# Kernel optimization log

Measured on AMD Instinct MI355X. Metric: run time of the kernel, lower is better.

Reference implementation:

```python
import jax, jax.numpy as jnp
import numpy as np

B, NMASK, DIM, HEADS = 8, 1024, 768, 12
HEAD_DIM = DIM // HEADS
SCALE = HEAD_DIM ** -0.5
NEG = -1e9  # finite stand-in for -inf to keep fully-masked rows NaN-free


def setup_inputs() -> dict:
    key = jax.random.key(0)
    ks = jax.random.split(key, 7)
    x = jax.random.normal(ks[0], (B, NMASK + 1, DIM), dtype=jnp.float32)
    # valid-prefix padding mask (realistic variable-length batch), lengths >= 1
    lengths = jax.random.randint(ks[1], (B,), 1, NMASK + 1)
    mask = jnp.arange(NMASK)[None, :] < lengths[:, None]  # (B, NMASK) bool
    w_qkv = jax.random.normal(ks[2], (DIM, 3 * DIM), dtype=jnp.float32) * (DIM ** -0.5)
    b_qkv = jax.random.normal(ks[3], (3 * DIM,), dtype=jnp.float32) * 0.02
    w_proj = jax.random.normal(ks[4], (DIM, DIM), dtype=jnp.float32) * (DIM ** -0.5)
    b_proj = jax.random.normal(ks[5], (DIM,), dtype=jnp.float32) * 0.02
    return {"x": x, "mask": mask, "w_qkv": w_qkv, "b_qkv": b_qkv,
            "w_proj": w_proj, "b_proj": b_proj}


def reference(x, mask, w_qkv, b_qkv, w_proj, b_proj):
    b, n, _ = x.shape
    qkv = x @ w_qkv + b_qkv                        # (b, n, 3*dim)
    qkv = qkv.reshape(b, n, 3, HEADS, HEAD_DIM)    # 'b n (qkv h d)'
    qkv = jnp.transpose(qkv, (2, 0, 3, 1, 4))      # (3, b, h, n, d)
    q, k, v = qkv[0], qkv[1], qkv[2]
    logits = jnp.einsum('bhid,bhjd->bhij', q, k) * SCALE
    m = jnp.pad(mask, ((0, 0), (1, 0)), constant_values=True)   # prepend CLS=True
    am = m[:, None, :] & m[:, :, None]             # (b, n, n)
    logits = jnp.where(am[:, None, :, :], logits, NEG)
    attn = jax.nn.softmax(logits, axis=-1)
    out = jnp.einsum('bhij,bhjd->bhid', attn, v)   # (b, h, n, d)
    out = jnp.transpose(out, (0, 2, 1, 3)).reshape(b, n, DIM)
    return out @ w_proj + b_proj                   # dropout is identity (eval/p=0)
```

## Files before the change

kernel.cpp:

```cpp
#include <hip/hip_runtime.h>
#include <stdint.h>

#define BATCH   8
#define NMASK_  1024
#define SEQ     1025
#define NPAD    1056
#define DIM     768
#define HEADS   12
#define HD      64
#define BHN     (BATCH*HEADS)
#define MROWS   (BATCH*SEQ)
#define K3      (3*DIM)

typedef unsigned short u16;
typedef __attribute__((ext_vector_type(8))) short s8v;
typedef __attribute__((ext_vector_type(4))) float f4v;
typedef __attribute__((ext_vector_type(4))) unsigned short u16x4;

__device__ __forceinline__ u16 rne_bf16(float f) {
  unsigned u = __float_as_uint(f);
  u += 0x7fffu + ((u >> 16) & 1u);
  return (u16)(u >> 16);
}
__device__ __forceinline__ float bf2f(u16 u) {
  return __uint_as_float(((unsigned)u) << 16);
}

__device__ __forceinline__ void gld16(const u16* g, u16* l) {
  __builtin_amdgcn_global_load_lds(
      (const __attribute__((address_space(1))) void*)g,
      (__attribute__((address_space(3))) void*)l, 16, 0, 0);
}

__global__ __launch_bounds__(256) void k_len(const int* __restrict__ mask,
                                             int* __restrict__ lens) {
  int b = blockIdx.x, t = threadIdx.x;
  int s = 0;
  for (int j = t; j < NMASK_; j += 256) s += (mask[b * NMASK_ + j] != 0) ? 1 : 0;
  __shared__ int red[256];
  red[t] = s; __syncthreads();
  for (int st = 128; st > 0; st >>= 1) { if (t < st) red[t] += red[t + st]; __syncthreads(); }
  if (t == 0) lens[b] = red[0] + 1;
}

__global__ __launch_bounds__(256) void k_cvt_x(const float* __restrict__ x,
                                               u16* __restrict__ xb, int n4) {
  int i = blockIdx.x * 256 + threadIdx.x;
  if (i >= n4) return;
  float4 v = ((const float4*)x)[i];
  u16x4 o;
  o[0] = rne_bf16(v.x); o[1] = rne_bf16(v.y); o[2] = rne_bf16(v.z); o[3] = rne_bf16(v.w);
  *(u16x4*)&xb[i * 4] = o;
}

__global__ __launch_bounds__(256) void k_wT(const float* __restrict__ w,
                                            u16* __restrict__ wT, int R, int C) {
  __shared__ float tile[32][33];
  int c0 = blockIdx.x * 32, r0 = blockIdx.y * 32;
  int tx = threadIdx.x & 31, ty = threadIdx.x >> 5;
  #pragma unroll
  for (int i = 0; i < 32; i += 8) tile[ty + i][tx] = w[(size_t)(r0 + ty + i) * C + c0 + tx];
  __syncthreads();
  #pragma unroll
  for (int i = 0; i < 32; i += 8)
    wT[(size_t)(c0 + ty + i) * R + r0 + tx] = rne_bf16(tile[tx][ty + i]);
}

__global__ __launch_bounds__(256) void k_zpad(u16* __restrict__ VT) {
  int idx = blockIdx.x * 256 + threadIdx.x;
  const int PADW = NPAD - SEQ;
  if (idx >= BHN * HD * PADW) return;
  int c = idx % PADW, rd = idx / PADW;
  VT[(size_t)rd * NPAD + SEQ + c] = 0;
}

__device__ __forceinline__ void gemm_ml128(const u16* __restrict__ A,
                                           const u16* __restrict__ Bt,
                                           int M, int m0, int n0,
                                           f4v acc[4][4], u16* smem) {
  u16* lA = smem;
  u16* lB = smem + 4096;
  const int t = threadIdx.x;
  const int w = t >> 6, l = t & 63, lg = l >> 4, lr = l & 15;
  const int wr = w >> 1, wc = w & 1;

  int rA0 = m0 + (t >> 2);       if (rA0 >= M) rA0 = M - 1;
  int rA1 = m0 + (t >> 2) + 64;  if (rA1 >= M) rA1 = M - 1;
  const u16* sA0 = A  + (size_t)rA0 * DIM + (t & 3) * 8;
  const u16* sA1 = A  + (size_t)rA1 * DIM + (t & 3) * 8;
  const u16* sB0 = Bt + (size_t)(n0 + (t >> 2)) * DIM + (t & 3) * 8;
  const u16* sB1 = Bt + (size_t)(n0 + (t >> 2) + 64) * DIM + (t & 3) * 8;
  u16* dA0 = &lA[w * 512];
  u16* dA1 = &lA[2048 + w * 512];
  u16* dB0 = &lB[w * 512];
  u16* dB1 = &lB[2048 + w * 512];

  #pragma unroll
  for (int fm = 0; fm < 4; fm++)
    #pragma unroll
    for (int fn = 0; fn < 4; fn++) { f4v z = {0.f, 0.f, 0.f, 0.f}; acc[fm][fn] = z; }

  for (int k0 = 0; k0 < DIM; k0 += 32) {
    __syncthreads();
    gld16(sA0, dA0); gld16(sA1, dA1);
    gld16(sB0, dB0); gld16(sB1, dB1);
    sA0 += 32; sA1 += 32; sB0 += 32; sB1 += 32;
    __syncthreads();
    s8v a[4], bb[4];
    #pragma unroll
    for (int fm = 0; fm < 4; fm++) a[fm] = *(const s8v*)&lA[(wr * 64 + fm * 16 + lr) * 32 + lg * 8];
    #pragma unroll
    for (int fn = 0; fn < 4; fn++) bb[fn] = *(const s8v*)&lB[(wc * 64 + fn * 16 + lr) * 32 + lg * 8];
    #pragma unroll
    for (int fm = 0; fm < 4; fm++)
      #pragma unroll
      for (int fn = 0; fn < 4; fn++)
        acc[fm][fn] = __builtin_amdgcn_mfma_f32_16x16x32_bf16(a[fm], bb[fn], acc[fm][fn], 0, 0, 0);
  }
}

__global__ __launch_bounds__(256) void k_gemm_qkv(const u16* __restrict__ xb,
                                                  const u16* __restrict__ wqkvT,
                                                  const float* __restrict__ bqkv,
                                                  const int* __restrict__ lens,
                                                  u16* __restrict__ Q,
                                                  u16* __restrict__ Kb,
                                                  u16* __restrict__ VT) {
  __shared__ alignas(16) u16 smem[16384];
  int m0 = blockIdx.x * 128, n0 = blockIdx.y * 128;
  const int which = n0 / DIM;
  if (which < 2) {
    int b0 = m0 / SEQ, off = m0 - b0 * SEQ;
    bool spans = (m0 + 127) >= (b0 + 1) * SEQ;
    if (!spans && off >= lens[b0]) return;
  }
  f4v acc[4][4];
  gemm_ml128(xb, wqkvT, MROWS, m0, n0, acc, smem);
  const int t = threadIdx.x;
  const int w = t >> 6, l = t & 63, lg = l >> 4, lr = l & 15;
  const int wr = w >> 1, wc = w & 1;
  const int hbase = (n0 - which * DIM) >> 6;
  const float qs = (which == 0) ? 0.125f : 1.0f;

  __syncthreads();
  #pragma unroll
  for (int fn = 0; fn < 4; fn++) {
    int col = wc * 64 + fn * 16 + lr;
    float bias = bqkv[n0 + col];
    #pragma unroll
    for (int fm = 0; fm < 4; fm++)
      #pragma unroll
      for (int r = 0; r < 4; r++) {
        int row = wr * 64 + fm * 16 + lg * 4 + r;
        smem[row * 128 + col] = rne_bf16((acc[fm][fn][r] + bias) * qs);
      }
  }
  __syncthreads();

  if (which < 2) {
    u16* dst = (which == 0) ? Q : Kb;
    #pragma unroll
    for (int p = 0; p < 8; p++) {
      int c = p * 256 + t;
      int row = c >> 4, col = (c & 15) * 8;
      int gm = m0 + row;
      if (gm >= MROWS) continue;
      int b = gm / SEQ, n = gm - b * SEQ;
      int head = hbase + (col >> 6), d = col & 63;
      *(s8v*)&dst[((size_t)(b * HEADS + head) * NPAD + n) * HD + d] =
          *(const s8v*)&smem[row * 128 + col];
    }
  } else {
    #pragma unroll
    for (int p = 0; p < 8; p++) {
      int c = p * 256 + t;
      int d = c & 127, nb = c >> 7;
      int gm0 = m0 + nb * 8;
      if (gm0 >= MROWS) continue;
      int head = hbase + (d >> 6), dl = d & 63;
      int b0 = gm0 / SEQ;
      if (gm0 + 7 < MROWS && (gm0 + 7) < (b0 + 1) * SEQ) {
        s8v v;
        #pragma unroll
        for (int e = 0; e < 8; e++) v[e] = (short)smem[(nb * 8 + e) * 128 + d];
        int n = gm0 - b0 * SEQ;
        *(s8v*)&VT[((size_t)(b0 * HEADS + head) * HD + dl) * NPAD + n] = v;
      } else {
        for (int e = 0; e < 8; e++) {
          int gm = gm0 + e;
          if (gm >= MROWS) break;
          int b = gm / SEQ, n = gm - b * SEQ;
          VT[((size_t)(b * HEADS + head) * HD + dl) * NPAD + n] = smem[(nb * 8 + e) * 128 + d];
        }
      }
    }
  }
}

__global__ __launch_bounds__(256) void k_vmean(const u16* __restrict__ VT,
                                               float* __restrict__ vmean) {
  int bh = blockIdx.x, t = threadIdx.x;
  int d = t >> 2, part = t & 3;
  const u16* row = VT + (size_t)(bh * HD + d) * NPAD;
  float s = 0.f;
  for (int jc = part * 264; jc < part * 264 + 264; jc += 8) {
    if (jc + 8 <= SEQ) {
      s8v v = *(const s8v*)&row[jc];
      #pragma unroll
      for (int e = 0; e < 8; e++) s += bf2f((u16)v[e]);
    } else {
      for (int e = 0; e < 8; e++) if (jc + e < SEQ) s += bf2f(row[jc + e]);
    }
  }
  __shared__ float red[256];
  red[t] = s; __syncthreads();
  if (part == 0)
    vmean[bh * HD + d] = (red[t] + red[t + 1] + red[t + 2] + red[t + 3]) * (1.0f / (float)SEQ);
}

__global__ __launch_bounds__(256) void k_vproj(const float* __restrict__ vmean,
                                               const u16* __restrict__ wprojT,
                                               const float* __restrict__ bproj,
                                               float* __restrict__ vproj) {
  int gid = blockIdx.x * 4 + (threadIdx.x >> 6);
  if (gid >= BATCH * DIM) return;
  int b = gid / DIM, n = gid - b * DIM;
  int l = threadIdx.x & 63;
  const u16* wr = wprojT + (size_t)n * DIM;
  const float* vm = vmean + b * DIM;
  float s = 0.f;
  #pragma unroll
  for (int i = 0; i < DIM / 64; ++i)
    s += vm[l + i * 64] * bf2f(wr[l + i * 64]);
  #pragma unroll
  for (int off = 32; off >= 1; off >>= 1) s += __shfl_xor(s, off);
  if (l == 0) vproj[gid] = s + bproj[n];
}

__global__ __launch_bounds__(256) void k_attn(const u16* __restrict__ Q,
                                              const u16* __restrict__ Kb,
                                              const u16* __restrict__ VT,
                                              const int* __restrict__ lens,
                                              u16* __restrict__ aout) {
  int bh = blockIdx.x; int b = bh / HEADS, h = bh - b * HEADS;
  int Lp1 = lens[b];
  int q0 = blockIdx.y * 64;
  if (q0 >= Lp1) return;
  __shared__ alignas(16) u16 Kt[64 * 64];
  __shared__ alignas(16) u16 Vt[64 * 64];
  __shared__ alignas(16) u16 Pt[4][16 * 72];
  const int t = threadIdx.x, w = t >> 6, l = t & 63, lg = l >> 4, lr = l & 15;
  const u16* Qbh = Q  + (size_t)bh * NPAD * HD;
  const u16* Kbh = Kb + (size_t)bh * NPAD * HD;
  const u16* Vbh = VT + (size_t)bh * HD * NPAD;

  int qi = q0 + w * 16 + lr;
  s8v qf[2];
  qf[0] = *(const s8v*)&Qbh[(size_t)qi * HD +      lg * 8];
  qf[1] = *(const s8v*)&Qbh[(size_t)qi * HD + 32 + lg * 8];

  f4v o[4];
  #pragma unroll
  for (int fd = 0; fd < 4; fd++) { f4v z = {0.f, 0.f, 0.f, 0.f}; o[fd] = z; }
  float ssacc[4];
  #pragma unroll
  for (int r = 0; r < 4; r++) ssacc[r] = 0.f;

  const int js = t >> 2, cs = t & 3;
  const u16* kSrc = Kbh + (size_t)js * HD   + cs * 8;
  const u16* vSrc = Vbh + (size_t)js * NPAD + cs * 8;
  const int kDst0 = js * 64 + ((cs       ^ (js & 7)) * 8);
  const int kDst1 = js * 64 + (((cs + 4) ^ (js & 7)) * 8);
  s8v kr0, kr1, vr0, vr1;
  kr0 = *(const s8v*)(kSrc);        kr1 = *(const s8v*)(kSrc + 32);
  vr0 = *(const s8v*)(vSrc);        vr1 = *(const s8v*)(vSrc + 32);

  for (int j0 = 0; j0 < Lp1; j0 += 64) {
    __syncthreads();
    *(s8v*)&Kt[kDst0] = kr0;  *(s8v*)&Kt[kDst1] = kr1;
    *(s8v*)&Vt[kDst0] = vr0;  *(s8v*)&Vt[kDst1] = vr1;
    if (j0 + 64 < Lp1) {
      kr0 = *(const s8v*)(kSrc + (size_t)(j0 + 64) * HD);
      kr1 = *(const s8v*)(kSrc + (size_t)(j0 + 64) * HD + 32);
      vr0 = *(const s8v*)(vSrc + (j0 + 64));
      vr1 = *(const s8v*)(vSrc + (j0 + 64) + 32);
    }
    __syncthreads();

    f4v sf[4];
    #pragma unroll
    for (int jf = 0; jf < 4; jf++) { f4v z = {0.f,0.f,0.f,0.f}; sf[jf] = z; }
    __builtin_amdgcn_s_setprio(1);
    #pragma unroll
    for (int jf = 0; jf < 4; jf++) {
      int j = jf * 16 + lr;
      #pragma unroll
      for (int kf = 0; kf < 2; kf++) {
        s8v kfr = *(const s8v*)&Kt[j * 64 + (((kf * 4 + lg) ^ (j & 7)) * 8)];
        sf[jf] = __builtin_amdgcn_mfma_f32_16x16x32_bf16(qf[kf], kfr, sf[jf], 0, 0, 0);
      }
    }
    __builtin_amdgcn_s_setprio(0);

    u16* P = &Pt[w][0];
    if (j0 + 64 <= Lp1) {
      #pragma unroll
      for (int r = 0; r < 4; r++) {
        float e0 = __expf(sf[0][r]);
        float e1 = __expf(sf[1][r]);
        float e2 = __expf(sf[2][r]);
        float e3 = __expf(sf[3][r]);
        int prow = (lg * 4 + r) * 72;
        P[prow +      lr] = rne_bf16(e0);
        P[prow + 16 + lr] = rne_bf16(e1);
        P[prow + 32 + lr] = rne_bf16(e2);
        P[prow + 48 + lr] = rne_bf16(e3);
        ssacc[r] += (e0 + e1) + (e2 + e3);
      }
    } else {
      bool ok[4];
      #pragma unroll
      for (int jf = 0; jf < 4; jf++) ok[jf] = (j0 + jf * 16 + lr) < Lp1;
      #pragma unroll
      for (int r = 0; r < 4; r++) {
        float e0 = __expf(ok[0] ? sf[0][r] : -1e30f);
        float e1 = __expf(ok[1] ? sf[1][r] : -1e30f);
        float e2 = __expf(ok[2] ? sf[2][r] : -1e30f);
        float e3 = __expf(ok[3] ? sf[3][r] : -1e30f);
        int prow = (lg * 4 + r) * 72;
        P[prow +      lr] = rne_bf16(e0);
        P[prow + 16 + lr] = rne_bf16(e1);
        P[prow + 32 + lr] = rne_bf16(e2);
        P[prow + 48 + lr] = rne_bf16(e3);
        ssacc[r] += (e0 + e1) + (e2 + e3);
      }
    }
    asm volatile("s_waitcnt lgkmcnt(0)" ::: "memory");
    s8v pa[2];
    pa[0] = *(const s8v*)&P[lr * 72 +      lg * 8];
    pa[1] = *(const s8v*)&P[lr * 72 + 32 + lg * 8];
    __builtin_amdgcn_s_setprio(1);
    #pragma unroll
    for (int fd = 0; fd < 4; fd++) {
      int dv = fd * 16 + lr;
      #pragma unroll
      for (int kf = 0; kf < 2; kf++) {
        s8v vb = *(const s8v*)&Vt[dv * 64 + (((kf * 4 + lg) ^ (dv & 7)) * 8)];
        o[fd] = __builtin_amdgcn_mfma_f32_16x16x32_bf16(pa[kf], vb, o[fd], 0, 0, 0);
      }
    }
    __builtin_amdgcn_s_setprio(0);
  }

  float inv[4];
  #pragma unroll
  for (int r = 0; r < 4; r++) {
    float rs = ssacc[r];
    rs += __shfl_xor(rs, 1); rs += __shfl_xor(rs, 2);
    rs += __shfl_xor(rs, 4); rs += __shfl_xor(rs, 8);
    inv[r] = 1.0f / rs;
  }
  #pragma unroll
  for (int fd = 0; fd < 4; fd++)
    #pragma unroll
    for (int r = 0; r < 4; r++) {
      int i = q0 + w * 16 + lg * 4 + r;
      if (i < Lp1)
        aout[(size_t)(b * SEQ + i) * DIM + h * HD + fd * 16 + lr] = rne_bf16(o[fd][r] * inv[r]);
    }
}

__global__ __launch_bounds__(256) void k_bcast(const int* __restrict__ lens,
                                               const float* __restrict__ vproj,
                                               float* __restrict__ out) {
  int idx = blockIdx.x * 256 + threadIdx.x;
  if (idx >= MROWS * DIM / 4) return;
  int e4 = idx * 4;
  int b = e4 / (SEQ * DIM);
  int rem = e4 - b * (SEQ * DIM);
  int i = rem / DIM;
  if (i >= lens[b]) {
    int c = rem - i * DIM;
    const float* vp = &vproj[b * DIM + c];
    float4 v = { vp[0], vp[1], vp[2], vp[3] };
    ((float4*)out)[idx] = v;
  }
}

__global__ __launch_bounds__(256) void k_gemm_proj(const u16* __restrict__ aout,
                                                   const u16* __restrict__ wprojT,
                                                   const float* __restrict__ bproj,
                                                   const int* __restrict__ lens,
                                                   float* __restrict__ out) {
  __shared__ alignas(16) u16 smem[16384];
  int m0 = blockIdx.x * 128, n0 = blockIdx.y * 128;
  {
    int b0 = m0 / SEQ, off = m0 - b0 * SEQ;
    bool spans = (m0 + 127) >= (b0 + 1) * SEQ;
    if (!spans && off >= lens[b0]) return;
  }
  f4v acc[4][4];
  gemm_ml128(aout, wprojT, MROWS, m0, n0, acc, smem);
  const int t = threadIdx.x;
  const int w = t >> 6, l = t & 63, lg = l >> 4, lr = l & 15;
  const int wr = w >> 1, wc = w & 1;
  #pragma unroll
  for (int fn = 0; fn < 4; fn++) {
    int gc = n0 + wc * 64 + fn * 16 + lr;
    float bias = bproj[gc];
    #pragma unroll
    for (int fm = 0; fm < 4; fm++)
      #pragma unroll
      for (int r = 0; r < 4; r++) {
        int gm = m0 + wr * 64 + fm * 16 + lg * 4 + r;
        if (gm < MROWS) out[(size_t)gm * DIM + gc] = acc[fm][fn][r] + bias;
      }
  }
}

extern "C" void kernel_launch(void* const* d_in, const int* in_sizes, int n_in,
                              void* d_out, int out_size, void* d_ws, size_t ws_size,
                              hipStream_t stream) {
  const float* x      = (const float*)d_in[0];
  const int*   mask   = (const int*)  d_in[1];
  const float* w_qkv  = (const float*)d_in[2];
  const float* b_qkv  = (const float*)d_in[3];
  const float* w_proj = (const float*)d_in[4];
  const float* b_proj = (const float*)d_in[5];
  float* out = (float*)d_out;

  u16* xb     = (u16*)d_ws;
  u16* wqkvT  = xb    + (size_t)MROWS * DIM;
  u16* wprojT = wqkvT + (size_t)K3 * DIM;
  u16* Q      = wprojT + (size_t)DIM * DIM;
  u16* Kb     = Q     + (size_t)BHN * NPAD * HD;
  u16* VT     = Kb    + (size_t)BHN * NPAD * HD;
  float* vmean = (float*)(VT + (size_t)BHN * NPAD * HD);
  int* lens    = (int*)(vmean + BHN * HD);
  float* vproj = (float*)(lens + 256);
  u16* aout   = xb;

  k_len  <<<dim3(BATCH), dim3(256), 0, stream>>>(mask, lens);
  k_cvt_x<<<dim3((MROWS * DIM / 4 + 255) / 256), dim3(256), 0, stream>>>(x, xb, MROWS * DIM / 4);
  k_wT   <<<dim3(K3 / 32, DIM / 32), dim3(256), 0, stream>>>(w_qkv, wqkvT, DIM, K3);
  k_wT   <<<dim3(DIM / 32, DIM / 32), dim3(256), 0, stream>>>(w_proj, wprojT, DIM, DIM);
  k_zpad <<<dim3((BHN * HD * (NPAD - SEQ) + 255) / 256), dim3(256), 0, stream>>>(VT);
  k_gemm_qkv<<<dim3((MROWS + 127) / 128, K3 / 128), dim3(256), 0, stream>>>(xb, wqkvT, b_qkv, lens, Q, Kb, VT);
  k_vmean<<<dim3(BHN), dim3(256), 0, stream>>>(VT, vmean);
  k_vproj<<<dim3((BATCH * DIM + 3) / 4), dim3(256), 0, stream>>>(vmean, wprojT, b_proj, vproj);
  k_attn <<<dim3(BHN, (SEQ + 63) / 64), dim3(256), 0, stream>>>(Q, Kb, VT, lens, aout);
  k_gemm_proj<<<dim3((MROWS + 127) / 128, DIM / 128), dim3(256), 0, stream>>>(aout, wprojT, b_proj, lens, out);
  k_bcast<<<dim3((MROWS * DIM / 4 + 255) / 256), dim3(256), 0, stream>>>(lens, vproj, out);
}
```

Before: 163.5 us.

## Double-buffer LDS tiles in shared GEMM with async prefetch of next K tile

The 128x128 GEMM helper now splits shared memory into two buffers per operand. It issues global-to-LDS loads for the next 32-wide K tile before computing on the current one, and uses explicit vmcnt waits and raw s_barrier calls instead of two __syncthreads per iteration. The aim is to overlap global memory latency with MFMA work in the QKV and projection GEMMs. It relies on the smem array holding 16K elements, and it hand-manages the wait counts, which is fragile if the compiler reorders loads.

```diff
diff --git a/kernel.cpp b/kernel.cpp
--- a/kernel.cpp
+++ b/kernel.cpp
@@ -32,6 +32,12 @@
       (__attribute__((address_space(3))) void*)l, 16, 0, 0);
 }
 
+__device__ __forceinline__ void barrier_() {
+  asm volatile("" ::: "memory");
+  __builtin_amdgcn_s_barrier();
+  asm volatile("" ::: "memory");
+}
+
 __global__ __launch_bounds__(256) void k_len(const int* __restrict__ mask,
                                              int* __restrict__ lens) {
   int b = blockIdx.x, t = threadIdx.x;
@@ -78,8 +84,6 @@
                                            const u16* __restrict__ Bt,
                                            int M, int m0, int n0,
                                            f4v acc[4][4], u16* smem) {
-  u16* lA = smem;
-  u16* lB = smem + 4096;
   const int t = threadIdx.x;
   const int w = t >> 6, l = t & 63, lg = l >> 4, lr = l & 15;
   const int wr = w >> 1, wc = w & 1;
@@ -90,22 +94,32 @@
   const u16* sA1 = A  + (size_t)rA1 * DIM + (t & 3) * 8;
   const u16* sB0 = Bt + (size_t)(n0 + (t >> 2)) * DIM + (t & 3) * 8;
   const u16* sB1 = Bt + (size_t)(n0 + (t >> 2) + 64) * DIM + (t & 3) * 8;
-  u16* dA0 = &lA[w * 512];
-  u16* dA1 = &lA[2048 + w * 512];
-  u16* dB0 = &lB[w * 512];
-  u16* dB1 = &lB[2048 + w * 512];
+  const int dO0 = w * 512, dO1 = 2048 + w * 512;
 
   #pragma unroll
   for (int fm = 0; fm < 4; fm++)
     #pragma unroll
     for (int fn = 0; fn < 4; fn++) { f4v z = {0.f, 0.f, 0.f, 0.f}; acc[fm][fn] = z; }
 
-  for (int k0 = 0; k0 < DIM; k0 += 32) {
-    __syncthreads();
-    gld16(sA0, dA0); gld16(sA1, dA1);
-    gld16(sB0, dB0); gld16(sB1, dB1);
-    sA0 += 32; sA1 += 32; sB0 += 32; sB1 += 32;
-    __syncthreads();
+  gld16(sA0, &smem[dO0]);        gld16(sA1, &smem[dO1]);
+  gld16(sB0, &smem[8192 + dO0]); gld16(sB1, &smem[8192 + dO1]);
+
+  const int NT = DIM / 32;
+  for (int kt = 0; kt < NT; ++kt) {
+    const int p = kt & 1;
+    if (kt + 1 < NT) {
+      const int ka = (kt + 1) * 32;
+      const int nb = (p ^ 1) * 4096;
+      gld16(sA0 + ka, &smem[nb + dO0]);        gld16(sA1 + ka, &smem[nb + dO1]);
+      gld16(sB0 + ka, &smem[8192 + nb + dO0]); gld16(sB1 + ka, &smem[8192 + nb + dO1]);
+      asm volatile("s_waitcnt vmcnt(4)" ::: "memory");
+    } else {
+      asm volatile("s_waitcnt vmcnt(0)" ::: "memory");
+    }
+    __builtin_amdgcn_sched_barrier(0);
+    barrier_();
+    const u16* lA = &smem[p * 4096];
+    const u16* lB = &smem[8192 + p * 4096];
     s8v a[4], bb[4];
     #pragma unroll
     for (int fm = 0; fm < 4; fm++) a[fm] = *(const s8v*)&lA[(wr * 64 + fm * 16 + lr) * 32 + lg * 8];
@@ -116,6 +130,7 @@
       #pragma unroll
       for (int fn = 0; fn < 4; fn++)
         acc[fm][fn] = __builtin_amdgcn_mfma_f32_16x16x32_bf16(a[fm], bb[fn], acc[fm][fn], 0, 0, 0);
+    barrier_();
   }
 }
 
```

Result: faster. 159.5 us, median of 2 (-2.4%).
